# Kernel tuning notes

Hardware: AMD Instinct MI355X
Metric: run time of the kernel (lower is better)

The kernel has to match this reference:

```python
import jax, jax.numpy as jnp
import numpy as np

N_HEADS = 16
D_MODEL = 1024
HEAD_DIM = D_MODEL // N_HEADS
MASK_FILL = -1e8  # matches torch masked_fill value -100000000.0


def setup_inputs() -> dict:
    key = jax.random.key(0)
    ks = jax.random.split(key, 12)
    B, L, P = 2, 2048, 2048
    s = 1.0 / np.sqrt(D_MODEL).astype(np.float32)
    inp = {
        "q": jax.random.normal(ks[0], (B, L, D_MODEL), dtype=jnp.float32),
        "k": jax.random.normal(ks[1], (B, P, D_MODEL), dtype=jnp.float32),
        "v": jax.random.normal(ks[2], (B, P, D_MODEL), dtype=jnp.float32),
        "attention_mask": jnp.ones((B, P), dtype=bool),
        "Wq": jax.random.normal(ks[3], (D_MODEL, D_MODEL), dtype=jnp.float32) * s,
        "bq": jnp.zeros((D_MODEL,), dtype=jnp.float32),
        "Wk": jax.random.normal(ks[4], (D_MODEL, D_MODEL), dtype=jnp.float32) * s,
        "bk": jnp.zeros((D_MODEL,), dtype=jnp.float32),
        "Wv": jax.random.normal(ks[5], (D_MODEL, D_MODEL), dtype=jnp.float32) * s,
        "bv": jnp.zeros((D_MODEL,), dtype=jnp.float32),
        "Wo": jax.random.normal(ks[6], (D_MODEL, D_MODEL), dtype=jnp.float32) * s,
        "bo": jnp.zeros((D_MODEL,), dtype=jnp.float32),
    }
    return inp


def _split_heads(x):
    # [B, S, D] -> [B, n, S, h]
    B, S, _ = x.shape
    return x.reshape(B, S, N_HEADS, HEAD_DIM).transpose(0, 2, 1, 3)


def reference(q, k, v, attention_mask, Wq, bq, Wk, bk, Wv, bv, Wo, bo):
    # Linear projections (torch Linear: x @ W.T + b)
    qm = _split_heads(q @ Wq.T + bq)
    km = _split_heads(k @ Wk.T + bk)
    vm = _split_heads(v @ Wv.T + bv)
    # scores: [B, n, L, P]
    scores = jnp.einsum('bnlh,bnph->bnlp', qm, km) / np.sqrt(HEAD_DIM).astype(np.float32)
    # mask [B, P] -> [B, 1, 1, P]; fill False positions with -1e8 (as in torch source)
    mask = attention_mask[:, None, None, :]
    scores = jnp.where(mask, scores, MASK_FILL)
    attn = jax.nn.softmax(scores, axis=-1)
    # dropout is identity in eval mode
    out = jnp.einsum('bnlp,bnph->bnlh', attn, vm)
    B, _, L, _ = out.shape
    out = out.transpose(0, 2, 1, 3).reshape(B, L, D_MODEL)
    return out @ Wo.T + bo
```

## Files before the change

kernel.cpp:

```cpp
#include <hip/hip_runtime.h>
#include <hip/hip_bf16.h>

typedef __attribute__((ext_vector_type(8))) __bf16 bf16x8;
typedef __attribute__((ext_vector_type(4))) float f32x4;
typedef __attribute__((ext_vector_type(16))) float f32x16;
typedef __attribute__((ext_vector_type(4))) unsigned short u16x4;
typedef __attribute__((ext_vector_type(2))) unsigned int u32x2;

#define LOG2E 1.4426950408889634f
#define FIXED_MAX 32.0f

__device__ __forceinline__ unsigned short f2bf(float f) {
  union { float f; unsigned int u; } x;
  x.f = f;
  unsigned int u = x.u;
  u += 0x7fffu + ((u >> 16) & 1u);
  return (unsigned short)(u >> 16);
}

__device__ __forceinline__ float fexp2(float x) {
  float r;
  asm("v_exp_f32 %0, %1" : "=v"(r) : "v"(x));
  return r;
}

__device__ __forceinline__ unsigned int cvtpk_bf16(float lo, float hi) {
  unsigned int r;
  asm("v_cvt_pk_bf16_f32 %0, %1, %2" : "=v"(r) : "v"(lo), "v"(hi));
  return r;
}

__device__ __forceinline__ void plswap(unsigned int& a, unsigned int& b) {
  auto r = __builtin_amdgcn_permlane32_swap((int)a, (int)b, false, false);
  a = (unsigned int)r[0];
  b = (unsigned int)r[1];
}

__device__ __forceinline__ void gload_lds16(const void* gsrc, void* lds) {
  __builtin_amdgcn_global_load_lds(
      (const __attribute__((address_space(1))) unsigned int*)gsrc,
      (__attribute__((address_space(3))) unsigned int*)lds, 16, 0, 0);
}

__global__ __launch_bounds__(256) void cvt_all(
    const float* __restrict__ q, const float* __restrict__ k, const float* __restrict__ v,
    const float* __restrict__ w0, const float* __restrict__ w1,
    const float* __restrict__ w2, const float* __restrict__ w3,
    unsigned short* __restrict__ qb, unsigned short* __restrict__ kb,
    unsigned short* __restrict__ vb, unsigned short* __restrict__ w0b,
    unsigned short* __restrict__ w1b, unsigned short* __restrict__ w2b,
    unsigned short* __restrict__ w3b) {
  long idx = (long)blockIdx.x * 256 + threadIdx.x;
  const long QV = 1024L * 1024;
  const long WQ = 256L * 1024;
  const float* src;
  unsigned short* dst;
  long base;
  if (idx < QV)                { src = q;  dst = qb;  base = idx; }
  else if (idx < 2 * QV)       { src = k;  dst = kb;  base = idx - QV; }
  else if (idx < 3 * QV)       { src = v;  dst = vb;  base = idx - 2 * QV; }
  else if (idx < 3 * QV + WQ)  { src = w0; dst = w0b; base = idx - 3 * QV; }
  else if (idx < 3 * QV + 2*WQ){ src = w1; dst = w1b; base = idx - 3 * QV - WQ; }
  else if (idx < 3 * QV + 3*WQ){ src = w2; dst = w2b; base = idx - 3 * QV - 2 * WQ; }
  else                         { src = w3; dst = w3b; base = idx - 3 * QV - 3 * WQ; }
  f32x4 val = *(const f32x4*)(src + base * 4);
  u16x4 o;
#pragma unroll
  for (int i = 0; i < 4; ++i) o[i] = f2bf(val[i]);
  *(u16x4*)(dst + base * 4) = o;
}

template <int MODE>
__global__ __launch_bounds__(256) void gemm_bt(
    const unsigned short* A0, const unsigned short* A1, const unsigned short* A2,
    const unsigned short* W0, const unsigned short* W1, const unsigned short* W2,
    const float* b0, const float* b1, const float* b2,
    void* o0, void* o1, void* o2) {
  __shared__ char smem[32768];
  constexpr int BM = (MODE == 1) ? 64 : 128;
  constexpr int NF = (MODE == 1) ? 2 : 4;
  const int z = blockIdx.z;
  const unsigned short* __restrict__ A = (z == 0) ? A0 : (z == 1) ? A1 : A2;
  const unsigned short* __restrict__ W = (z == 0) ? W0 : (z == 1) ? W1 : W2;
  const float* __restrict__ bias = (z == 0) ? b0 : (z == 1) ? b1 : b2;
  void* __restrict__ out = (z == 0) ? o0 : (z == 1) ? o1 : o2;
  const float oscale = (MODE == 0 && z == 0) ? 0.125f * LOG2E : 1.0f;
  const bool kblocked = (MODE == 0 && z == 1);

  const int tid = threadIdx.x;
  const int lane = tid & 63;
  const int wave = tid >> 6;
  const int wm = (MODE == 1) ? 0 : (wave >> 1) * 64;
  const int wn = (MODE == 1) ? wave * 32 : (wave & 1) * 64;
  const int bm0 = blockIdx.x * BM;
  const int bn0 = blockIdx.y * 128;
  const int K = 1024;
  const int srow = tid >> 2;
  const int sg = tid & 3;

  f32x4 acc[4][NF] = {};

  auto stageA = [&](int kt, int buf) {
    char* dst = smem + buf * 8192;
#pragma unroll
    for (int h = 0; h < BM / 64; ++h) {
      int row = srow + h * 64;
      int gs = sg ^ ((row >> 1) & 3);
      gload_lds16((const char*)(A + (long)(bm0 + row) * K + kt * 32) + gs * 16,
                  dst + h * 4096 + tid * 16);
    }
  };
  auto stageB = [&](int kt, int buf) {
    char* dst = smem + 16384 + buf * 8192;
#pragma unroll
    for (int h = 0; h < 2; ++h) {
      int row = srow + h * 64;
      int gs = sg ^ ((row >> 1) & 3);
      gload_lds16((const char*)(W + (long)(bn0 + row) * K + kt * 32) + gs * 16,
                  dst + h * 4096 + tid * 16);
    }
  };

  stageA(0, 0);
  stageB(0, 0);
  __syncthreads();

  const int nk = K / 32;
  for (int kt = 0; kt < nk; ++kt) {
    const int cur = kt & 1;
    if (kt + 1 < nk) { stageA(kt + 1, cur ^ 1); stageB(kt + 1, cur ^ 1); }
    char* curA = smem + cur * 8192;
    char* curB = smem + 16384 + cur * 8192;
    const int kb = (lane >> 4) * 16;
    bf16x8 af[4], bfr[NF];
#pragma unroll
    for (int i = 0; i < 4; ++i) {
      int row = wm + i * 16 + (lane & 15);
      af[i] = *(const bf16x8*)(curA + row * 64 + (kb ^ (((row >> 1) & 3) << 4)));
    }
#pragma unroll
    for (int j = 0; j < NF; ++j) {
      int row = wn + j * 16 + (lane & 15);
      bfr[j] = *(const bf16x8*)(curB + row * 64 + (kb ^ (((row >> 1) & 3) << 4)));
    }
#pragma unroll
    for (int i = 0; i < 4; ++i)
#pragma unroll
      for (int j = 0; j < NF; ++j)
        acc[i][j] = __builtin_amdgcn_mfma_f32_16x16x32_bf16(af[i], bfr[j], acc[i][j], 0, 0, 0);
    __syncthreads();
  }

#pragma unroll
  for (int i = 0; i < 4; ++i) {
#pragma unroll
    for (int j = 0; j < NF; ++j) {
#pragma unroll
      for (int r = 0; r < 4; ++r) {
        int row = bm0 + wm + i * 16 + (lane >> 4) * 4 + r;
        int col = bn0 + wn + j * 16 + (lane & 15);
        float vv = (acc[i][j][r] + bias[col]) * oscale;
        if (MODE == 0) {
          int bb = row >> 11, ll = row & 2047;
          int hh = col >> 6, hd = col & 63;
          long idx;
          if (kblocked) {
            int pt = ll >> 6, p = ll & 63, g = hd >> 3, e = hd & 7;
            idx = ((((long)((bb * 16 + hh) * 32 + pt)) * 8 + g) * 64 + p) * 8 + e;
          } else {
            idx = (((long)(bb * 16 + hh) * 2048 + ll) << 6) + hd;
          }
          ((unsigned short*)out)[idx] = f2bf(vv);
        } else {
          ((float*)out)[(long)row * 1024 + col] = vv;
        }
      }
    }
  }
}

__global__ __launch_bounds__(256) void transpose_v(const unsigned short* __restrict__ Vm,
                                                   unsigned short* __restrict__ Vt) {
  __shared__ unsigned short t[64][68];
  const int bh = blockIdx.y;
  const int pt = blockIdx.x;
  const int p0 = pt * 64;
  const int tid = threadIdx.x;
#pragma unroll
  for (int it = 0; it < 4; ++it) {
    int idx = it * 256 + tid;
    int r = idx >> 4;
    int c4 = (idx & 15) * 4;
    *(u16x4*)&t[r][c4] = *(const u16x4*)(Vm + ((long)bh * 2048 + p0 + r) * 64 + c4);
  }
  __syncthreads();
#pragma unroll
  for (int it = 0; it < 4; ++it) {
    int idx = it * 256 + tid;
    int hd = idx >> 4;
    int pp4 = (idx & 15) * 4;
    int g = pp4 >> 3, e0 = pp4 & 7;
    u16x4 v;
#pragma unroll
    for (int j = 0; j < 4; ++j) v[j] = t[pp4 + j][hd];
    *(u16x4*)(Vt + ((((long)(bh * 32 + pt)) * 8 + g) * 64 + hd) * 8 + e0) = v;
  }
}

__global__ __launch_bounds__(256, 4) void attn_fwd(
    const unsigned short* __restrict__ Qm,
    const unsigned short* __restrict__ Kblk,
    const unsigned short* __restrict__ Vblk,
    const int* __restrict__ mask,
    unsigned short* __restrict__ ao) {
  __shared__ char smem[37504];
  char* const Kl = smem;
  char* const Vl = smem + 16384;
  unsigned short* const maskb = (unsigned short*)(smem + 32768);
  float* const lsums = (float*)(smem + 36864);
  int* const allm = (int*)(smem + 37376);

  const int tid = threadIdx.x, lane = tid & 63, wave = tid >> 6;
  const int kv = wave & 1;
  const int qg = wave >> 1;
  const int h2 = lane >> 5;
  const int ql = lane & 31;
  const int orig = blockIdx.y * 32 + blockIdx.x;
  const int wgid = (orig & 7) * 128 + (orig >> 3);
  const int bh = wgid >> 5, b = bh >> 4, hh = bh & 15;
  const int q0 = (wgid & 31) * 64;
  const unsigned short* Qbase = Qm + ((long)bh * 2048 + q0 + qg * 32) * 64;
  const char* Kg = (const char*)(Kblk + (long)bh * 2048 * 64);
  const char* Vg = (const char*)(Vblk + (long)bh * 2048 * 64);

  auto stage_pair = [&](int s) {
#pragma unroll
    for (int c = 0; c < 4; ++c) {
      int off = (c * 256 + tid) * 16;
      gload_lds16(Kg + (long)s * 16384 + off, Kl + off);
      gload_lds16(Vg + (long)s * 16384 + off, Vl + off);
    }
  };

  stage_pair(0);

  {
    const int* mrow = mask + b * 2048;
    int p8 = tid * 8;
    int ok = 1;
#pragma unroll
    for (int i = 0; i < 4; ++i) {
      int m0 = mrow[p8 + 2 * i];
      int m1 = mrow[p8 + 2 * i + 1];
      ok &= (m0 != 0) & (m1 != 0);
      unsigned int lo = m0 ? 0u : 1u;
      unsigned int hi = m1 ? 0u : 1u;
      *(unsigned int*)(maskb + p8 + 2 * i) = lo | (hi << 16);
    }
    unsigned long long bal = __ballot(ok != 0);
    if (lane < 8) allm[wave * 8 + lane] = (int)(((bal >> (lane * 8)) & 0xFFull) == 0xFFull);
  }

  bf16x8 qf[4];
#pragma unroll
  for (int ks = 0; ks < 4; ++ks)
    qf[ks] = *(const bf16x8*)(Qbase + (long)ql * 64 + ks * 16 + h2 * 8);

  f32x16 o0 = {}, o1 = {};
  float lsum = 0.f;
  const char* const Kc = Kl + kv * 8192;
  const char* const Vc = Vl + kv * 8192;
  __syncthreads();

  for (int s = 0; s < 16; ++s) {
    const int pt = 2 * s + kv;

    f32x16 s0 = {}, s1 = {};
#pragma unroll
    for (int ks = 0; ks < 4; ++ks) {
      int gl = ks * 2 + h2;
      bf16x8 k0 = *(const bf16x8*)(Kc + gl * 1024 + ql * 16);
      bf16x8 k1 = *(const bf16x8*)(Kc + gl * 1024 + 512 + ql * 16);
      s0 = __builtin_amdgcn_mfma_f32_32x32x16_bf16(k0, qf[ks], s0, 0, 0, 0);
      s1 = __builtin_amdgcn_mfma_f32_32x32x16_bf16(k1, qf[ks], s1, 0, 0, 0);
    }

    if (!allm[pt]) {
#pragma unroll
      for (int rq = 0; rq < 4; ++rq) {
        u16x4 m0 = *(const u16x4*)(maskb + pt * 64 + rq * 8 + 4 * h2);
        u16x4 m1 = *(const u16x4*)(maskb + pt * 64 + 32 + rq * 8 + 4 * h2);
#pragma unroll
        for (int i = 0; i < 4; ++i) {
          s0[rq * 4 + i] = m0[i] ? -1.0e8f : s0[rq * 4 + i];
          s1[rq * 4 + i] = m1[i] ? -1.0e8f : s1[rq * 4 + i];
        }
      }
    }

#pragma unroll
    for (int i = 0; i < 16; ++i) {
      float p = fexp2(s0[i] - FIXED_MAX);
      s0[i] = p; lsum += p;
    }
#pragma unroll
    for (int i = 0; i < 16; ++i) {
      float p = fexp2(s1[i] - FIXED_MAX);
      s1[i] = p; lsum += p;
    }

    bf16x8 pa[4];
    {
      union { unsigned int w[4]; bf16x8 v; } u;
      unsigned int w0, w1, w2, w3;
      w0 = cvtpk_bf16(s0[0],  s0[1]);  w1 = cvtpk_bf16(s0[2],  s0[3]);
      w2 = cvtpk_bf16(s0[4],  s0[5]);  w3 = cvtpk_bf16(s0[6],  s0[7]);
      plswap(w0, w2); plswap(w1, w3);
      u.w[0] = w0; u.w[1] = w1; u.w[2] = w2; u.w[3] = w3; pa[0] = u.v;
      w0 = cvtpk_bf16(s0[8],  s0[9]);  w1 = cvtpk_bf16(s0[10], s0[11]);
      w2 = cvtpk_bf16(s0[12], s0[13]); w3 = cvtpk_bf16(s0[14], s0[15]);
      plswap(w0, w2); plswap(w1, w3);
      u.w[0] = w0; u.w[1] = w1; u.w[2] = w2; u.w[3] = w3; pa[1] = u.v;
      w0 = cvtpk_bf16(s1[0],  s1[1]);  w1 = cvtpk_bf16(s1[2],  s1[3]);
      w2 = cvtpk_bf16(s1[4],  s1[5]);  w3 = cvtpk_bf16(s1[6],  s1[7]);
      plswap(w0, w2); plswap(w1, w3);
      u.w[0] = w0; u.w[1] = w1; u.w[2] = w2; u.w[3] = w3; pa[2] = u.v;
      w0 = cvtpk_bf16(s1[8],  s1[9]);  w1 = cvtpk_bf16(s1[10], s1[11]);
      w2 = cvtpk_bf16(s1[12], s1[13]); w3 = cvtpk_bf16(s1[14], s1[15]);
      plswap(w0, w2); plswap(w1, w3);
      u.w[0] = w0; u.w[1] = w1; u.w[2] = w2; u.w[3] = w3; pa[3] = u.v;
    }

#pragma unroll
    for (int kb = 0; kb < 4; ++kb) {
      int gl = kb * 2 + h2;
      bf16x8 v0 = *(const bf16x8*)(Vc + gl * 1024 + ql * 16);
      bf16x8 v1 = *(const bf16x8*)(Vc + gl * 1024 + 512 + ql * 16);
      o0 = __builtin_amdgcn_mfma_f32_32x32x16_bf16(v0, pa[kb], o0, 0, 0, 0);
      o1 = __builtin_amdgcn_mfma_f32_32x32x16_bf16(v1, pa[kb], o1, 0, 0, 0);
    }

    __syncthreads();
    if (s + 1 < 16) {
      stage_pair(s + 1);
      __syncthreads();
    }
  }

  float lf = lsum + __shfl_xor(lsum, 32);
  if (kv == 1) {
    char* Oc = smem + qg * 16384;
#pragma unroll
    for (int rq = 0; rq < 4; ++rq) {
      f32x4 w0 = {o0[rq*4+0], o0[rq*4+1], o0[rq*4+2], o0[rq*4+3]};
      int d4 = (rq * 8 + 4 * h2) * 4;
      *(f32x4*)(Oc + ql * 256 + (d4 ^ ((ql & 7) << 5))) = w0;
      f32x4 w1 = {o1[rq*4+0], o1[rq*4+1], o1[rq*4+2], o1[rq*4+3]};
      int d41 = 128 + d4;
      *(f32x4*)(Oc + ql * 256 + (d41 ^ ((ql & 7) << 5))) = w1;
    }
    if (h2 == 0) lsums[qg * 64 + ql] = lf;
  }
  __syncthreads();
  if (kv == 0) {
    const char* Oc = smem + qg * 16384;
#pragma unroll
    for (int rq = 0; rq < 4; ++rq) {
      int d4 = (rq * 8 + 4 * h2) * 4;
      f32x4 w0 = *(const f32x4*)(Oc + ql * 256 + (d4 ^ ((ql & 7) << 5)));
      f32x4 w1 = *(const f32x4*)(Oc + ql * 256 + ((128 + d4) ^ ((ql & 7) << 5)));
#pragma unroll
      for (int i = 0; i < 4; ++i) { o0[rq*4+i] += w0[i]; o1[rq*4+i] += w1[i]; }
    }
    lf += lsums[qg * 64 + ql];
    float inv = 1.0f / lf;
    unsigned short* aop = ao + ((long)(b * 2048 + q0 + qg * 32 + ql) << 10) + hh * 64;
#pragma unroll
    for (int rq = 0; rq < 4; ++rq) {
      unsigned int lo = cvtpk_bf16(o0[rq * 4 + 0] * inv, o0[rq * 4 + 1] * inv);
      unsigned int hi = cvtpk_bf16(o0[rq * 4 + 2] * inv, o0[rq * 4 + 3] * inv);
      u32x2 st = {lo, hi};
      *(u32x2*)(aop + rq * 8 + 4 * h2) = st;
    }
#pragma unroll
    for (int rq = 0; rq < 4; ++rq) {
      unsigned int lo = cvtpk_bf16(o1[rq * 4 + 0] * inv, o1[rq * 4 + 1] * inv);
      unsigned int hi = cvtpk_bf16(o1[rq * 4 + 2] * inv, o1[rq * 4 + 3] * inv);
      u32x2 st = {lo, hi};
      *(u32x2*)(aop + 32 + rq * 8 + 4 * h2) = st;
    }
  }
}

extern "C" void kernel_launch(void* const* d_in, const int* in_sizes, int n_in,
                              void* d_out, int out_size, void* d_ws, size_t ws_size,
                              hipStream_t stream) {
  const float* q = (const float*)d_in[0];
  const float* k = (const float*)d_in[1];
  const float* v = (const float*)d_in[2];
  const int* mask = (const int*)d_in[3];
  const float* Wq = (const float*)d_in[4];
  const float* bq = (const float*)d_in[5];
  const float* Wk = (const float*)d_in[6];
  const float* bk = (const float*)d_in[7];
  const float* Wv = (const float*)d_in[8];
  const float* bv = (const float*)d_in[9];
  const float* Wo = (const float*)d_in[10];
  const float* bo = (const float*)d_in[11];

  char* ws = (char*)d_ws;
  unsigned short* qb  = (unsigned short*)(ws + (0L << 20));
  unsigned short* kb  = (unsigned short*)(ws + (8L << 20));
  unsigned short* vb  = (unsigned short*)(ws + (16L << 20));
  unsigned short* wqb = (unsigned short*)(ws + (24L << 20));
  unsigned short* wkb = (unsigned short*)(ws + (26L << 20));
  unsigned short* wvb = (unsigned short*)(ws + (28L << 20));
  unsigned short* wob = (unsigned short*)(ws + (30L << 20));
  unsigned short* Qh  = (unsigned short*)(ws + (32L << 20));
  unsigned short* Kb  = (unsigned short*)(ws + (40L << 20));
  unsigned short* Vh  = (unsigned short*)(ws + (48L << 20));
  unsigned short* Vb  = (unsigned short*)(ws + (56L << 20));
  unsigned short* aob = (unsigned short*)(ws + (64L << 20));

  cvt_all<<<16384, 256, 0, stream>>>(q, k, v, Wq, Wk, Wv, Wo,
                                     qb, kb, vb, wqb, wkb, wvb, wob);
  gemm_bt<0><<<dim3(32, 8, 3), 256, 0, stream>>>(qb, kb, vb, wqb, wkb, wvb,
                                                 bq, bk, bv, Qh, Kb, Vh);
  transpose_v<<<dim3(32, 32), 256, 0, stream>>>(Vh, Vb);
  attn_fwd<<<dim3(32, 32), 256, 0, stream>>>(Qh, Kb, Vb, mask, aob);
  gemm_bt<1><<<dim3(64, 8, 1), 256, 0, stream>>>(aob, aob, aob, wob, wob, wob,
                                                 bo, bo, bo, d_out, d_out, d_out);
  (void)in_sizes; (void)n_in; (void)out_size; (void)ws_size;
}
```

Before: 128.9 us.

## Fuse V transpose into projection epilogue, add L2 prefetch and MFMA priority

The V projection epilogue now writes directly into the blocked, transposed layout that attention consumes, so the separate transpose_v kernel launch and its extra read/write pass are removed. The attention loop also issues a 4-byte global_load_lds touch of the next K/V tile into a dummy LDS slot, to warm L2 ahead of the real staging, and raises wave priority around the MFMA blocks with s_setprio. The scattered 2-byte stores in the V epilogue may be less coalesced than before, and the prefetch adds extra memory instructions each iteration.

```diff
diff --git a/kernel.cpp b/kernel.cpp
--- a/kernel.cpp
+++ b/kernel.cpp
@@ -40,6 +40,12 @@
   __builtin_amdgcn_global_load_lds(
       (const __attribute__((address_space(1))) unsigned int*)gsrc,
       (__attribute__((address_space(3))) unsigned int*)lds, 16, 0, 0);
+}
+
+__device__ __forceinline__ void l2touch(const void* gsrc, void* dummy_lds) {
+  __builtin_amdgcn_global_load_lds(
+      (const __attribute__((address_space(1))) unsigned int*)gsrc,
+      (__attribute__((address_space(3))) unsigned int*)dummy_lds, 4, 0, 0);
 }
 
 __global__ __launch_bounds__(256) void cvt_all(
@@ -85,7 +91,6 @@
   const float* __restrict__ bias = (z == 0) ? b0 : (z == 1) ? b1 : b2;
   void* __restrict__ out = (z == 0) ? o0 : (z == 1) ? o1 : o2;
   const float oscale = (MODE == 0 && z == 0) ? 0.125f * LOG2E : 1.0f;
-  const bool kblocked = (MODE == 0 && z == 1);
 
   const int tid = threadIdx.x;
   const int lane = tid & 63;
@@ -164,9 +169,12 @@
           int bb = row >> 11, ll = row & 2047;
           int hh = col >> 6, hd = col & 63;
           long idx;
-          if (kblocked) {
-            int pt = ll >> 6, p = ll & 63, g = hd >> 3, e = hd & 7;
-            idx = ((((long)((bb * 16 + hh) * 32 + pt)) * 8 + g) * 64 + p) * 8 + e;
+          if (z == 1) {
+            idx = ((((long)((bb * 16 + hh) * 32 + (ll >> 6))) * 8 + (hd >> 3)) * 64
+                   + (ll & 63)) * 8 + (hd & 7);
+          } else if (z == 2) {
+            idx = ((((long)((bb * 16 + hh) * 32 + (ll >> 6))) * 8 + ((ll >> 3) & 7)) * 64
+                   + hd) * 8 + (ll & 7);
           } else {
             idx = (((long)(bb * 16 + hh) * 2048 + ll) << 6) + hd;
           }
@@ -179,46 +187,19 @@
   }
 }
 
-__global__ __launch_bounds__(256) void transpose_v(const unsigned short* __restrict__ Vm,
-                                                   unsigned short* __restrict__ Vt) {
-  __shared__ unsigned short t[64][68];
-  const int bh = blockIdx.y;
-  const int pt = blockIdx.x;
-  const int p0 = pt * 64;
-  const int tid = threadIdx.x;
-#pragma unroll
-  for (int it = 0; it < 4; ++it) {
-    int idx = it * 256 + tid;
-    int r = idx >> 4;
-    int c4 = (idx & 15) * 4;
-    *(u16x4*)&t[r][c4] = *(const u16x4*)(Vm + ((long)bh * 2048 + p0 + r) * 64 + c4);
-  }
-  __syncthreads();
-#pragma unroll
-  for (int it = 0; it < 4; ++it) {
-    int idx = it * 256 + tid;
-    int hd = idx >> 4;
-    int pp4 = (idx & 15) * 4;
-    int g = pp4 >> 3, e0 = pp4 & 7;
-    u16x4 v;
-#pragma unroll
-    for (int j = 0; j < 4; ++j) v[j] = t[pp4 + j][hd];
-    *(u16x4*)(Vt + ((((long)(bh * 32 + pt)) * 8 + g) * 64 + hd) * 8 + e0) = v;
-  }
-}
-
 __global__ __launch_bounds__(256, 4) void attn_fwd(
     const unsigned short* __restrict__ Qm,
     const unsigned short* __restrict__ Kblk,
     const unsigned short* __restrict__ Vblk,
     const int* __restrict__ mask,
     unsigned short* __restrict__ ao) {
-  __shared__ char smem[37504];
+  __shared__ char smem[37760];
   char* const Kl = smem;
   char* const Vl = smem + 16384;
   unsigned short* const maskb = (unsigned short*)(smem + 32768);
   float* const lsums = (float*)(smem + 36864);
   int* const allm = (int*)(smem + 37376);
+  char* const dummy = smem + 37504;
 
   const int tid = threadIdx.x, lane = tid & 63, wave = tid >> 6;
   const int kv = wave & 1;
@@ -273,9 +254,15 @@
   __syncthreads();
 
   for (int s = 0; s < 16; ++s) {
+    if (s + 1 < 16) {
+      const char* tb = (tid < 128) ? (Kg + (long)(s + 1) * 16384 + (tid & 127) * 128)
+                                   : (Vg + (long)(s + 1) * 16384 + (tid & 127) * 128);
+      l2touch(tb, dummy);
+    }
     const int pt = 2 * s + kv;
 
     f32x16 s0 = {}, s1 = {};
+    __builtin_amdgcn_s_setprio(1);
 #pragma unroll
     for (int ks = 0; ks < 4; ++ks) {
       int gl = ks * 2 + h2;
@@ -284,6 +271,7 @@
       s0 = __builtin_amdgcn_mfma_f32_32x32x16_bf16(k0, qf[ks], s0, 0, 0, 0);
       s1 = __builtin_amdgcn_mfma_f32_32x32x16_bf16(k1, qf[ks], s1, 0, 0, 0);
     }
+    __builtin_amdgcn_s_setprio(0);
 
     if (!allm[pt]) {
 #pragma unroll
@@ -331,6 +319,7 @@
       u.w[0] = w0; u.w[1] = w1; u.w[2] = w2; u.w[3] = w3; pa[3] = u.v;
     }
 
+    __builtin_amdgcn_s_setprio(1);
 #pragma unroll
     for (int kb = 0; kb < 4; ++kb) {
       int gl = kb * 2 + h2;
@@ -339,6 +328,7 @@
       o0 = __builtin_amdgcn_mfma_f32_32x32x16_bf16(v0, pa[kb], o0, 0, 0, 0);
       o1 = __builtin_amdgcn_mfma_f32_32x32x16_bf16(v1, pa[kb], o1, 0, 0, 0);
     }
+    __builtin_amdgcn_s_setprio(0);
 
     __syncthreads();
     if (s + 1 < 16) {
@@ -418,15 +408,13 @@
   unsigned short* wob = (unsigned short*)(ws + (30L << 20));
   unsigned short* Qh  = (unsigned short*)(ws + (32L << 20));
   unsigned short* Kb  = (unsigned short*)(ws + (40L << 20));
-  unsigned short* Vh  = (unsigned short*)(ws + (48L << 20));
   unsigned short* Vb  = (unsigned short*)(ws + (56L << 20));
   unsigned short* aob = (unsigned short*)(ws + (64L << 20));
 
   cvt_all<<<16384, 256, 0, stream>>>(q, k, v, Wq, Wk, Wv, Wo,
                                      qb, kb, vb, wqb, wkb, wvb, wob);
   gemm_bt<0><<<dim3(32, 8, 3), 256, 0, stream>>>(qb, kb, vb, wqb, wkb, wvb,
-                                                 bq, bk, bv, Qh, Kb, Vh);
-  transpose_v<<<dim3(32, 32), 256, 0, stream>>>(Vh, Vb);
+                                                 bq, bk, bv, Qh, Kb, Vb);
   attn_fwd<<<dim3(32, 32), 256, 0, stream>>>(Qh, Kb, Vb, mask, aob);
   gemm_bt<1><<<dim3(64, 8, 1), 256, 0, stream>>>(aob, aob, aob, wob, wob, wob,
                                                  bo, bo, bo, d_out, d_out, d_out);
```

Result: slower. 132.2 us (+2.6%).
